# Kernel optimization log

Hardware: AMD Instinct MI355X
Metric: run time of the kernel (lower is better)

The kernel has to match this reference:

```python
import jax, jax.numpy as jnp
import numpy as np

N, F_IN = 4096, 128
UNITS0, HEADS0 = 16, 4   # hidden GraphAttention layer
UNITS1, HEADS1 = 1, 1    # final layer (sigmoid, mean over last axis)


def _glorot(key, shape):
    fan_in, fan_out = shape[0], shape[1]
    std = (2.0 / (fan_in + fan_out)) ** 0.5
    return std * jax.random.normal(key, shape, dtype=jnp.float32)


def setup_inputs() -> dict:
    key = jax.random.key(0)
    ks = jax.random.split(key, 8)
    x = jax.random.normal(ks[0], (N, F_IN), dtype=jnp.float32)
    adj = (jax.random.uniform(ks[1], (N, N)) < 0.01).astype(jnp.float32)
    return {
        "x": x,
        "adj": adj,
        "w0": _glorot(ks[2], (F_IN, UNITS0)),
        "aw1_0": _glorot(ks[3], (UNITS0, HEADS0)),
        "aw2_0": _glorot(ks[4], (UNITS0, HEADS0)),
        "w1": _glorot(ks[5], (UNITS0 * HEADS0, UNITS1)),
        "aw1_1": _glorot(ks[6], (UNITS1, HEADS1)),
        "aw2_1": _glorot(ks[7], (UNITS1, HEADS1)),
    }


def _gat_layer(x, adj, w, aw1, aw2, activation, final_layer):
    h = x @ w                                   # [N, units]
    a1 = h @ aw1                                # [N, H]
    a2 = h @ aw2                                # [N, H]
    # relu(a1_i + a2_j) broadcast -> [N, N, H]
    coeffs = jax.nn.relu(a1[:, None, :] + a2[None, :, :])
    # elementwise adjacency mask then softmax over neighbor axis (axis=1),
    # matching tf.nn.softmax(adj * coeffs[:,:,i], axis=1)
    attn = jax.nn.softmax(adj[:, :, None] * coeffs, axis=1)   # [N, N, H]
    # per-head aggregation then concat heads: [N, H*units]
    out = jnp.einsum('ijh,jd->ihd', attn, h).reshape(h.shape[0], -1)
    if final_layer:
        out = out.mean(axis=-1)                 # [N]
    return activation(out)


def reference(x, adj, w0, aw1_0, aw2_0, w1, aw1_1, aw2_1):
    h = _gat_layer(x, adj, w0, aw1_0, aw2_0, jax.nn.relu, False)   # [N, 64]
    out = _gat_layer(h, adj, w1, aw1_1, aw2_1, jax.nn.sigmoid, True)  # [N]
    return out
```

## Files before the change

### kernel.cpp

```cpp
#include <hip/hip_runtime.h>
#include <hip/hip_bf16.h>

#define N 4096
#define FIN 128
#define U0 16
#define H0 4
#define MAXD 128
#define NGEMM (N / 16)

__global__ void k1_fused(const float* __restrict__ adj, const float* __restrict__ x,
                         const float* __restrict__ w0, const float* __restrict__ aw1,
                         const float* __restrict__ aw2,
                         int* __restrict__ deg, int* __restrict__ cols,
                         float* __restrict__ h0, float* __restrict__ a1,
                         float* __restrict__ a2, float* __restrict__ S0) {
    const int t = threadIdx.x;
    if (blockIdx.x < NGEMM) {
        const int bid = blockIdx.x;
        __shared__ float xs[16][FIN + 1];
        __shared__ float ws[FIN][U0];
        __shared__ float hs[16][U0 + 1];
        const int r0 = bid * 16;

        for (int k = t; k < FIN * U0; k += 256) ws[k / U0][k % U0] = w0[k];
        for (int k = t; k < 16 * FIN; k += 256)
            xs[k / FIN][k % FIN] = x[(size_t)(r0 + k / FIN) * FIN + (k % FIN)];
        __syncthreads();

        const int r = t / U0, u = t % U0;
        float acc = 0.f;
        #pragma unroll 8
        for (int k = 0; k < FIN; ++k) acc += xs[r][k] * ws[k][u];
        hs[r][u] = acc;
        h0[(size_t)(r0 + r) * U0 + u] = acc;
        __syncthreads();

        if (t < 16 * H0) {
            const int rr = t / H0, hh = t % H0;
            float s1 = 0.f, s2 = 0.f;
            #pragma unroll
            for (int u2 = 0; u2 < U0; ++u2) {
                float hv = hs[rr][u2];
                s1 += hv * aw1[u2 * H0 + hh];
                s2 += hv * aw2[u2 * H0 + hh];
            }
            a1[(r0 + rr) * H0 + hh] = s1;
            a2[(r0 + rr) * H0 + hh] = s2;
        } else if (t >= 128 && t < 144) {
            const int d = t - 128;
            float s = 0.f;
            #pragma unroll
            for (int rr = 0; rr < 16; ++rr) s += hs[rr][d];
            atomicAdd(&S0[d], s);
        }
    } else {
        const int row = blockIdx.x - NGEMM;
        const int lane = t & 63, wid = t >> 6;
        const float4* __restrict__ arow =
            reinterpret_cast<const float4*>(adj + (size_t)row * N);

        float4 v[4];
        int c = 0;
        #pragma unroll
        for (int p = 0; p < 4; ++p) {
            v[p] = arow[t + 256 * p];
            c += (v[p].x != 0.f) + (v[p].y != 0.f) + (v[p].z != 0.f) + (v[p].w != 0.f);
        }

        int sc = c;
        #pragma unroll
        for (int s = 1; s < 64; s <<= 1) {
            int u = __shfl_up(sc, s);
            if (lane >= s) sc += u;
        }
        __shared__ int wsum[4];
        if (lane == 63) wsum[wid] = sc;
        __syncthreads();
        int base = 0;
        #pragma unroll
        for (int w2 = 0; w2 < 4; ++w2)
            if (w2 < wid) base += wsum[w2];
        const int off = base + sc - c;
        if (t == 255) deg[row] = min(base + sc, MAXD);

        int w = row * MAXD + off;
        const int wend = row * MAXD + MAXD;
        #pragma unroll
        for (int p = 0; p < 4; ++p) {
            const int j0 = (t + 256 * p) * 4;
            if (v[p].x != 0.f && w < wend) cols[w++] = j0;
            if (v[p].y != 0.f && w < wend) cols[w++] = j0 + 1;
            if (v[p].z != 0.f && w < wend) cols[w++] = j0 + 2;
            if (v[p].w != 0.f && w < wend) cols[w++] = j0 + 3;
        }
    }
}

__global__ void attn0(const float* __restrict__ h0, const float* __restrict__ a1,
                      const float* __restrict__ a2, const float* __restrict__ S0,
                      const int* __restrict__ deg, const int* __restrict__ cols,
                      const float* __restrict__ w1,
                      float* __restrict__ hp, float* __restrict__ S1part) {
    const int i = blockIdx.x;
    const int t = threadIdx.x;
    __shared__ int cls[MAXD];
    __shared__ float ln[4][64];
    __shared__ float ld[4][64];

    const int dg = deg[i];
    if (t < MAXD) cls[t] = (t < dg) ? cols[(size_t)i * MAXD + t] : 0;
    __syncthreads();

    const int wid = t >> 6, lane = t & 63;
    const int hh = lane >> 4, d = lane & 15;
    const float a1v = a1[i * H0 + hh];

    float accn = 0.f, accd = 0.f;
    for (int c = 0; ; c += 4) {
        const int kb = wid + 4 * c;
        if (kb >= dg) break;
        int ja[4];
        float ms[4];
        #pragma unroll
        for (int q = 0; q < 4; ++q) {
            const int k = kb + 4 * q;
            ja[q] = cls[k < MAXD ? k : 0];
            ms[q] = (k < dg) ? 1.f : 0.f;
        }
        float a2v[4], h0v[4];
        #pragma unroll
        for (int q = 0; q < 4; ++q) {
            a2v[q] = a2[ja[q] * H0 + hh];
            h0v[q] = h0[(size_t)ja[q] * U0 + d];
        }
        #pragma unroll
        for (int q = 0; q < 4; ++q) {
            float cc = a1v + a2v[q];
            cc = cc > 0.f ? cc : 0.f;
            const float e = (__expf(cc) - 1.f) * ms[q];
            accn = fmaf(e, h0v[q], accn);
            accd += e;
        }
    }
    ln[wid][lane] = accn;
    ld[wid][lane] = accd;
    __syncthreads();

    if (t < 64) {
        const float an = ln[0][t] + ln[1][t] + ln[2][t] + ln[3][t];
        const float ad = ld[0][t] + ld[1][t] + ld[2][t] + ld[3][t];
        float o = (an + S0[t & 15]) / (ad + (float)N);
        o = o > 0.f ? o : 0.f;

        float pv = o * w1[t];
        #pragma unroll
        for (int off = 32; off; off >>= 1) pv += __shfl_down(pv, off);
        if (t == 0) {
            hp[i] = pv;
            atomicAdd(&S1part[i & 255], pv);
        }
    }
}

__global__ void attn1(const float* __restrict__ hp, const float* __restrict__ S1part,
                      const float* __restrict__ aw11, const float* __restrict__ aw21,
                      const int* __restrict__ deg, const int* __restrict__ cols,
                      float* __restrict__ out) {
    __shared__ float s1red[4];
    const int t = threadIdx.x;
    const int w = t >> 6, lane = t & 63;

    float s = S1part[t];
    #pragma unroll
    for (int o = 32; o; o >>= 1) s += __shfl_down(s, o);
    if (lane == 0) s1red[w] = s;
    __syncthreads();
    const float S1 = s1red[0] + s1red[1] + s1red[2] + s1red[3];

    const int i = blockIdx.x * 4 + w;
    const float w1v = aw11[0], w2v = aw21[0];
    const float a1v = hp[i] * w1v;
    const int dg = deg[i];
    const int* __restrict__ cl = cols + (size_t)i * MAXD;

    float accn = 0.f, accd = 0.f;
    for (int k = lane; k < dg; k += 64) {
        const int j = cl[k];
        const float hj = hp[j];
        float cc = a1v + hj * w2v;
        cc = cc > 0.f ? cc : 0.f;
        const float e = __expf(cc) - 1.f;
        accn = fmaf(e, hj, accn);
        accd += e;
    }
    #pragma unroll
    for (int o = 32; o; o >>= 1) {
        accn += __shfl_down(accn, o);
        accd += __shfl_down(accd, o);
    }
    if (lane == 0) {
        const float v = (accn + S1) / (accd + (float)N);
        out[i] = 1.f / (1.f + __expf(-v));
    }
}

extern "C" void kernel_launch(void* const* d_in, const int* in_sizes, int n_in,
                              void* d_out, int out_size, void* d_ws, size_t ws_size,
                              hipStream_t stream) {
    const float* x    = (const float*)d_in[0];
    const float* adj  = (const float*)d_in[1];
    const float* w0   = (const float*)d_in[2];
    const float* aw10 = (const float*)d_in[3];
    const float* aw20 = (const float*)d_in[4];
    const float* w1   = (const float*)d_in[5];
    const float* aw11 = (const float*)d_in[6];
    const float* aw21 = (const float*)d_in[7];
    float* out = (float*)d_out;

    char* p = (char*)d_ws;
    auto alloc = [&](size_t bytes) {
        char* r = p;
        p += (bytes + 255) & ~(size_t)255;
        return r;
    };
    float* S0     = (float*)alloc(256);
    float* S1part = (float*)alloc(1024);
    float* h0     = (float*)alloc((size_t)N * U0 * 4);
    float* a1     = (float*)alloc((size_t)N * H0 * 4);
    float* a2     = (float*)alloc((size_t)N * H0 * 4);
    float* hp     = (float*)alloc((size_t)N * 4);
    int*   deg    = (int*)alloc((size_t)N * 4);
    int*   cols   = (int*)alloc((size_t)N * MAXD * 4);

    hipMemsetAsync(S0, 0, 256 + 1024, stream);
    k1_fused<<<N + NGEMM, 256, 0, stream>>>(adj, x, w0, aw10, aw20,
                                            deg, cols, h0, a1, a2, S0);
    attn0<<<N, 256, 0, stream>>>(h0, a1, a2, S0, deg, cols, w1, hp, S1part);
    attn1<<<N / 4, 256, 0, stream>>>(hp, S1part, aw11, aw21, deg, cols, out);
}
```

Measured before the change: 37.30 us.

## Replace global atomics and memset with per-block partial sums and shared staging

Global atomic accumulations for the S0 and S1 sums are replaced by per-block partial arrays that consumer blocks reduce redundantly, which removes the memset launch. Column-index compaction in the adjacency pass now goes through shared memory and is written out coalesced. attn1 stages the whole hp vector and the per-row column lists in shared memory and computes the S1 sum itself. The trade is redundant reduction work in every attn0 and attn1 block: each attn0 block reads 4096 partials and each attn1 block reads all of hp. attn1 also now needs 16KB of shared memory per block.

```diff
diff --git a/kernel.cpp b/kernel.cpp
--- a/kernel.cpp
+++ b/kernel.cpp
@@ -13,7 +13,7 @@
                          const float* __restrict__ aw2,
                          int* __restrict__ deg, int* __restrict__ cols,
                          float* __restrict__ h0, float* __restrict__ a1,
-                         float* __restrict__ a2, float* __restrict__ S0) {
+                         float* __restrict__ a2, float* __restrict__ partS0) {
     const int t = threadIdx.x;
     if (blockIdx.x < NGEMM) {
         const int bid = blockIdx.x;
@@ -51,7 +51,7 @@
             float s = 0.f;
             #pragma unroll
             for (int rr = 0; rr < 16; ++rr) s += hs[rr][d];
-            atomicAdd(&S0[d], s);
+            partS0[bid * 16 + d] = s;
         }
     } else {
         const int row = blockIdx.x - NGEMM;
@@ -59,6 +59,10 @@
         const float4* __restrict__ arow =
             reinterpret_cast<const float4*>(adj + (size_t)row * N);
 
+        __shared__ int cls[MAXD];
+        __shared__ int wsum[4];
+        __shared__ int dgs;
+
         float4 v[4];
         int c = 0;
         #pragma unroll
@@ -73,7 +77,6 @@
             int u = __shfl_up(sc, s);
             if (lane >= s) sc += u;
         }
-        __shared__ int wsum[4];
         if (lane == 63) wsum[wid] = sc;
         __syncthreads();
         int base = 0;
@@ -81,34 +84,55 @@
         for (int w2 = 0; w2 < 4; ++w2)
             if (w2 < wid) base += wsum[w2];
         const int off = base + sc - c;
-        if (t == 255) deg[row] = min(base + sc, MAXD);
-
-        int w = row * MAXD + off;
-        const int wend = row * MAXD + MAXD;
+        if (t == 255) {
+            const int dgv = min(base + sc, MAXD);
+            dgs = dgv;
+            deg[row] = dgv;
+        }
+
+        int w = off;
         #pragma unroll
         for (int p = 0; p < 4; ++p) {
             const int j0 = (t + 256 * p) * 4;
-            if (v[p].x != 0.f && w < wend) cols[w++] = j0;
-            if (v[p].y != 0.f && w < wend) cols[w++] = j0 + 1;
-            if (v[p].z != 0.f && w < wend) cols[w++] = j0 + 2;
-            if (v[p].w != 0.f && w < wend) cols[w++] = j0 + 3;
-        }
+            if (v[p].x != 0.f && w < MAXD) cls[w++] = j0;
+            if (v[p].y != 0.f && w < MAXD) cls[w++] = j0 + 1;
+            if (v[p].z != 0.f && w < MAXD) cls[w++] = j0 + 2;
+            if (v[p].w != 0.f && w < MAXD) cls[w++] = j0 + 3;
+        }
+        __syncthreads();
+        if (t < dgs) cols[(size_t)row * MAXD + t] = cls[t];
     }
 }
 
 __global__ void attn0(const float* __restrict__ h0, const float* __restrict__ a1,
-                      const float* __restrict__ a2, const float* __restrict__ S0,
+                      const float* __restrict__ a2, const float* __restrict__ partS0,
                       const int* __restrict__ deg, const int* __restrict__ cols,
-                      const float* __restrict__ w1,
-                      float* __restrict__ hp, float* __restrict__ S1part) {
+                      const float* __restrict__ w1, float* __restrict__ hp) {
     const int i = blockIdx.x;
     const int t = threadIdx.x;
     __shared__ int cls[MAXD];
+    __shared__ float red[16][17];
+    __shared__ float s0s[16];
     __shared__ float ln[4][64];
     __shared__ float ld[4][64];
 
     const int dg = deg[i];
     if (t < MAXD) cls[t] = (t < dg) ? cols[(size_t)i * MAXD + t] : 0;
+
+    {
+        const int d = t & 15, ch = t >> 4;
+        float s = 0.f;
+        #pragma unroll
+        for (int k = ch; k < 256; k += 16) s += partS0[k * 16 + d];
+        red[ch][d] = s;
+    }
+    __syncthreads();
+    if (t < 16) {
+        float s2 = 0.f;
+        #pragma unroll
+        for (int k = 0; k < 16; ++k) s2 += red[k][t];
+        s0s[t] = s2;
+    }
     __syncthreads();
 
     const int wid = t >> 6, lane = t & 63;
@@ -116,8 +140,8 @@
     const float a1v = a1[i * H0 + hh];
 
     float accn = 0.f, accd = 0.f;
-    for (int c = 0; ; c += 4) {
-        const int kb = wid + 4 * c;
+    for (int c = 0; ; ++c) {
+        const int kb = wid + 16 * c;
         if (kb >= dg) break;
         int ja[4];
         float ms[4];
@@ -149,44 +173,53 @@
     if (t < 64) {
         const float an = ln[0][t] + ln[1][t] + ln[2][t] + ln[3][t];
         const float ad = ld[0][t] + ld[1][t] + ld[2][t] + ld[3][t];
-        float o = (an + S0[t & 15]) / (ad + (float)N);
+        float o = (an + s0s[t & 15]) / (ad + (float)N);
         o = o > 0.f ? o : 0.f;
 
         float pv = o * w1[t];
         #pragma unroll
         for (int off = 32; off; off >>= 1) pv += __shfl_down(pv, off);
-        if (t == 0) {
-            hp[i] = pv;
-            atomicAdd(&S1part[i & 255], pv);
-        }
-    }
-}
-
-__global__ void attn1(const float* __restrict__ hp, const float* __restrict__ S1part,
+        if (t == 0) hp[i] = pv;
+    }
+}
+
+__global__ void attn1(const float* __restrict__ hp,
                       const float* __restrict__ aw11, const float* __restrict__ aw21,
                       const int* __restrict__ deg, const int* __restrict__ cols,
                       float* __restrict__ out) {
+    __shared__ float hps[N];
+    __shared__ int cls[4][MAXD];
     __shared__ float s1red[4];
     const int t = threadIdx.x;
     const int w = t >> 6, lane = t & 63;
-
-    float s = S1part[t];
+    const int i0 = blockIdx.x * 4;
+
+    float s = 0.f;
+    const float4* __restrict__ hp4 = reinterpret_cast<const float4*>(hp);
+    #pragma unroll
+    for (int k = t; k < N / 4; k += 256) {
+        float4 v = hp4[k];
+        reinterpret_cast<float4*>(hps)[k] = v;
+        s += v.x + v.y + v.z + v.w;
+    }
+    for (int k = t; k < 4 * MAXD; k += 256)
+        cls[k >> 7][k & 127] = cols[(size_t)(i0 + (k >> 7)) * MAXD + (k & 127)];
+
     #pragma unroll
     for (int o = 32; o; o >>= 1) s += __shfl_down(s, o);
     if (lane == 0) s1red[w] = s;
     __syncthreads();
     const float S1 = s1red[0] + s1red[1] + s1red[2] + s1red[3];
 
-    const int i = blockIdx.x * 4 + w;
+    const int i = i0 + w;
     const float w1v = aw11[0], w2v = aw21[0];
-    const float a1v = hp[i] * w1v;
+    const float a1v = hps[i] * w1v;
     const int dg = deg[i];
-    const int* __restrict__ cl = cols + (size_t)i * MAXD;
 
     float accn = 0.f, accd = 0.f;
     for (int k = lane; k < dg; k += 64) {
-        const int j = cl[k];
-        const float hj = hp[j];
+        const int j = cls[w][k];
+        const float hj = hps[j];
         float cc = a1v + hj * w2v;
         cc = cc > 0.f ? cc : 0.f;
         const float e = __expf(cc) - 1.f;
@@ -223,8 +256,7 @@
         p += (bytes + 255) & ~(size_t)255;
         return r;
     };
-    float* S0     = (float*)alloc(256);
-    float* S1part = (float*)alloc(1024);
+    float* partS0 = (float*)alloc(NGEMM * 16 * 4);
     float* h0     = (float*)alloc((size_t)N * U0 * 4);
     float* a1     = (float*)alloc((size_t)N * H0 * 4);
     float* a2     = (float*)alloc((size_t)N * H0 * 4);
@@ -232,9 +264,8 @@
     int*   deg    = (int*)alloc((size_t)N * 4);
     int*   cols   = (int*)alloc((size_t)N * MAXD * 4);
 
-    hipMemsetAsync(S0, 0, 256 + 1024, stream);
     k1_fused<<<N + NGEMM, 256, 0, stream>>>(adj, x, w0, aw10, aw20,
-                                            deg, cols, h0, a1, a2, S0);
-    attn0<<<N, 256, 0, stream>>>(h0, a1, a2, S0, deg, cols, w1, hp, S1part);
-    attn1<<<N / 4, 256, 0, stream>>>(hp, S1part, aw11, aw21, deg, cols, out);
-}
+                                            deg, cols, h0, a1, a2, partS0);
+    attn0<<<N, 256, 0, stream>>>(h0, a1, a2, partS0, deg, cols, w1, hp);
+    attn1<<<N / 4, 256, 0, stream>>>(hp, aw11, aw21, deg, cols, out);
+}
```

Result: no change. 37.93 us (+1.7%).
